# Kernel optimization log

Measured on AMD Instinct MI355X. Metric: run time of the kernel, lower is better.

The kernel has to match this reference:

```python
import jax, jax.numpy as jnp
import numpy as np

B, L, D = 4, 4096, 1024
H = 16
DK = D // H  # 64
EPS = 1e-5


def setup_inputs() -> dict:
    key = jax.random.key(0)
    ks = jax.random.split(key, 9)
    s = 1.0 / np.sqrt(D)
    return {
        "Q": jax.random.normal(ks[0], (B, L, D), dtype=jnp.float32),
        "W_Q": jax.random.uniform(ks[1], (D, D), jnp.float32, -s, s),
        "b_Q": jax.random.uniform(ks[2], (D,), jnp.float32, -s, s),
        "W_K": jax.random.uniform(ks[3], (D, D), jnp.float32, -s, s),
        "b_K": jax.random.uniform(ks[4], (D,), jnp.float32, -s, s),
        "W_V": jax.random.uniform(ks[5], (D, D), jnp.float32, -s, s),
        "b_V": jax.random.uniform(ks[6], (D,), jnp.float32, -s, s),
        "W_O": jax.random.uniform(ks[7], (D, D), jnp.float32, -s, s),
        "b_O": jax.random.uniform(ks[8], (D,), jnp.float32, -s, s),
    }


def reference(Q, W_Q, b_Q, W_K, b_K, W_V, b_V, W_O, b_O):
    # Projections (torch Linear: x @ W.T + b). K = V = Q (self-attention).
    q = (Q @ W_Q.T + b_Q).reshape(B, L, H, DK)  # blhd
    k = (Q @ W_K.T + b_K).reshape(B, L, H, DK)
    v = (Q @ W_V.T + b_V).reshape(B, L, H, DK)

    phi_q = jax.nn.elu(q) + 1.0
    phi_k = jax.nn.elu(k) + 1.0

    # KV outer-product accumulation over sequence: [b,h,d,m]
    KV = jnp.einsum('blhd,blhm->bhdm', phi_k, v)
    K_sum = phi_k.sum(axis=1)                       # [b,h,d]
    Z = 1.0 / (jnp.einsum('blhd,bhd->blh', phi_q, K_sum) + EPS)
    V_new = jnp.einsum('blhd,bhdm->blhm', phi_q, KV) * Z[..., None]

    out = V_new.reshape(B, L, H * DK) @ W_O.T + b_O  # [b,L,d_model]
    return out
```

## Files before the change

kernel.cpp:

```cpp
#include <hip/hip_runtime.h>

typedef unsigned short u16;
typedef unsigned int   u32;
typedef __attribute__((ext_vector_type(8))) short short8;
typedef __attribute__((ext_vector_type(4))) float f32x4;
typedef __attribute__((ext_vector_type(4))) u16   u16x4;

#define NB 4
#define SL 4096
#define DM 1024
#define NH 16
#define DK 64

__device__ __forceinline__ u16 f2bf(float f) {
  u32 u = __builtin_bit_cast(u32, f);
  u = (u + 0x7fffu + ((u >> 16) & 1u)) >> 16;
  return (u16)u;
}
__device__ __forceinline__ float bf2f(u16 v) {
  u32 u = ((u32)v) << 16;
  return __builtin_bit_cast(float, u);
}
__device__ __forceinline__ float eluP1(float x) {
  return x > 0.f ? x + 1.f : __expf(x);
}
#define GLL(gp, lp) __builtin_amdgcn_global_load_lds(     \
    (const __attribute__((address_space(1))) void*)(gp),  \
    (__attribute__((address_space(3))) void*)(lp), 16, 0, 0)

__global__ void cvt_all(const float* __restrict__ Qf,
                        const float* __restrict__ WQ, const float* __restrict__ WK,
                        const float* __restrict__ WV, const float* __restrict__ WO,
                        const float* __restrict__ bQ, const float* __restrict__ bK,
                        const float* __restrict__ bV,
                        u16* __restrict__ Qbf, u16* __restrict__ Wqkv,
                        u16* __restrict__ Wobf, float* __restrict__ biasQKV) {
  int b = blockIdx.x, tid = threadIdx.x;
  if (b < 16384) {
    int i = b * 256 + tid;
    f32x4 f = *(const f32x4*)(Qf + (size_t)i * 4);
    u16x4 o = { f2bf(f[0]), f2bf(f[1]), f2bf(f[2]), f2bf(f[3]) };
    *(u16x4*)(Qbf + (size_t)i * 4) = o;
  } else if (b < 20480) {
    int r = (b - 16384) >> 10;
    int i = ((b - 16384) & 1023) * 256 + tid;
    const float* src = r == 0 ? WQ : r == 1 ? WK : r == 2 ? WV : WO;
    u16* dst = (r == 3) ? Wobf : Wqkv + (size_t)r * 1048576;
    f32x4 f = *(const f32x4*)(src + (size_t)i * 4);
    u16x4 o = { f2bf(f[0]), f2bf(f[1]), f2bf(f[2]), f2bf(f[3]) };
    *(u16x4*)(dst + (size_t)i * 4) = o;
  } else {
    int i = (b - 20480) * 256 + tid;
    if (i < 3072) {
      float v = (i < 1024) ? bQ[i] : (i < 2048) ? bK[i - 1024] : bV[i - 2048];
      biasQKV[i] = v;
    }
  }
}


#define VM8 asm volatile("s_waitcnt vmcnt(8)" ::: "memory")
#define NOP ((void)0)

#define SA(buf, ks, kt) do {                                      \
    const u16* g_ = Ag + (((kt) & 15) * 64 + (ks) * 32);          \
    u16* l_ = ldsA + (buf) * 32768 + (ks) * 8192;                 \
    GLL(g_, l_); GLL(g_ + 16 * 1024, l_ + 512); } while (0)

#define SB(buf, ks, kt) do {                                      \
    const u16* g_ = Wg + (((kt) & 15) * 64 + (ks) * 32);          \
    u16* l_ = ldsB + (buf) * 32768 + (ks) * 8192;                 \
    GLL(g_, l_); GLL(g_ + 16 * 1024, l_ + 512); } while (0)

#define LDB(buf, ks) do {                                         \
    const u16* pB_ = bBase + (buf) * 32768 + (ks) * 8192;         \
    bf0 = *(const short8*)(pB_ + bOff[0]);                        \
    bf1 = *(const short8*)(pB_ + bOff[1]);                        \
    bf2 = *(const short8*)(pB_ + bOff[2]);                        \
    bf3 = *(const short8*)(pB_ + bOff[3]); } while (0)

#define PHASE(buf, ks, tb, PRE, STG) do {                         \
    short8 af_[4];                                                \
    const u16* pA_ = aBase + (buf) * 32768 + (ks) * 8192;         \
    _Pragma("unroll") for (int t_ = 0; t_ < 4; t_++)              \
      af_[t_] = *(const short8*)(pA_ + aOff[(tb) + t_]);          \
    PRE;                                                          \
    STG;                                                          \
    VM8;                                                          \
    __builtin_amdgcn_s_barrier();                                 \
    asm volatile("s_waitcnt lgkmcnt(0)" ::: "memory");            \
    __builtin_amdgcn_s_setprio(1);                                \
    _Pragma("unroll") for (int t_ = 0; t_ < 4; t_++) {            \
      acc[(tb) + t_][0] = __builtin_amdgcn_mfma_f32_16x16x32_bf16(af_[t_], bf0, acc[(tb) + t_][0], 0, 0, 0); \
      acc[(tb) + t_][1] = __builtin_amdgcn_mfma_f32_16x16x32_bf16(af_[t_], bf1, acc[(tb) + t_][1], 0, 0, 0); \
      acc[(tb) + t_][2] = __builtin_amdgcn_mfma_f32_16x16x32_bf16(af_[t_], bf2, acc[(tb) + t_][2], 0, 0, 0); \
      acc[(tb) + t_][3] = __builtin_amdgcn_mfma_f32_16x16x32_bf16(af_[t_], bf3, acc[(tb) + t_][3], 0, 0, 0); \
    }                                                             \
    __builtin_amdgcn_s_setprio(0);                                \
  } while (0)

#define MAIN_8PHASE_LOOP                                          \
  SA(0, 0, 0); SB(0, 0, 0); SA(0, 1, 0); SB(0, 1, 0);             \
  SA(1, 0, 1); SB(1, 0, 1);                                       \
  VM8;                                                            \
  __builtin_amdgcn_s_barrier();                                   \
  asm volatile("" ::: "memory");                                  \
  _Pragma("unroll 1")                                             \
  for (int i = 0; i < 8; i++) {                                   \
    PHASE(0, 0, 0, LDB(0, 0), SB(1, 1, 2 * i + 1));               \
    PHASE(0, 0, 4, NOP,       SA(1, 1, 2 * i + 1));               \
    PHASE(0, 1, 0, LDB(0, 1), SB(0, 0, 2 * i + 2));               \
    PHASE(0, 1, 4, NOP,       SA(0, 0, 2 * i + 2));               \
    PHASE(1, 0, 0, LDB(1, 0), SB(0, 1, 2 * i + 2));               \
    PHASE(1, 0, 4, NOP,       SA(0, 1, 2 * i + 2));               \
    PHASE(1, 1, 0, LDB(1, 1), SB(1, 0, 2 * i + 3));               \
    PHASE(1, 1, 4, NOP,       SA(1, 0, 2 * i + 3));               \
  }

__global__ __launch_bounds__(512, 2) void gemm_qkv(const u16* __restrict__ A,
                                                   const u16* __restrict__ Wqkv,
                                                   const float* __restrict__ biasQKV,
                                                   u16* __restrict__ phiq,
                                                   u16* __restrict__ phiKT,
                                                   u16* __restrict__ vT) {
  const int K = 1024;
  const int bId = blockIdx.x;
  const int xcd = bId & 7, s = bId >> 3;
  const int tile_m = xcd * 8 + s / 12;
  const int tile_n = s % 12;
  const int region = tile_n >> 2;

  const int tid = threadIdx.x, lane = tid & 63, wv = tid >> 6;
  const int i16 = lane & 15, q = lane >> 4;
  const int waveM = wv >> 2, waveN = wv & 3;

  __shared__ u16 smem[65536];

  const int r0 = wv * 32 + (lane >> 2);
  const int kc = (lane & 3) ^ ((r0 >> 1) & 3);
  const u16* Ag = A + (size_t)(tile_m * 256 + r0) * K + kc * 8;
  const u16* Wg = Wqkv + (size_t)(tile_n * 256 + r0) * K + kc * 8;
  u16* ldsA = smem + wv * 1024;
  u16* ldsB = smem + 16384 + wv * 1024;

  const u16* aBase = (region == 0) ? smem + 16384 : smem;
  const u16* bBase = (region == 0) ? smem : smem + 16384;
  int aOff[8], bOff[4];
#pragma unroll
  for (int t = 0; t < 8; t++) {
    int m = waveM * 128 + t * 16 + i16;
    aOff[t] = m * 32 + ((q ^ ((m >> 1) & 3)) << 3);
  }
#pragma unroll
  for (int u = 0; u < 4; u++) {
    int n = waveN * 64 + u * 16 + i16;
    bOff[u] = n * 32 + ((q ^ ((n >> 1) & 3)) << 3);
  }

  f32x4 acc[8][4] = {};
  short8 bf0, bf1, bf2, bf3;

  MAIN_8PHASE_LOOP

  u16* T = smem;
  const int TS = 132;
  u16* dstT = (region == 1) ? phiKT : vT;
  const int bI = tile_m >> 4;
  const int lb = (tile_m & 15) * 256;

#pragma unroll
  for (int h = 0; h < 2; h++) {
    __syncthreads();
    if (waveM == h) {
      if (region == 0) {
#pragma unroll
        for (int t = 0; t < 8; t++) {
          f32x4 b4 = *(const f32x4*)(biasQKV + tile_n * 256 + h * 128 + t * 16 + q * 4);
#pragma unroll
          for (int u = 0; u < 4; u++) {
            int cC = waveN * 64 + u * 16 + i16;
            u16x4 o;
#pragma unroll
            for (int r = 0; r < 4; r++) o[r] = f2bf(eluP1(acc[t][u][r] + b4[r]));
            *(u16x4*)(T + cC * TS + t * 16 + q * 4) = o;
          }
        }
      } else {
#pragma unroll
        for (int u = 0; u < 4; u++) {
          int cC = waveN * 64 + u * 16 + i16;
          float bs = biasQKV[tile_n * 256 + cC];
#pragma unroll
          for (int t = 0; t < 8; t++) {
            u16x4 o;
#pragma unroll
            for (int r = 0; r < 4; r++) {
              float vv = acc[t][u][r] + bs;
              if (region == 1) vv = eluP1(vv);
              o[r] = f2bf(vv);
            }
            *(u16x4*)(T + cC * TS + t * 16 + q * 4) = o;
          }
        }
      }
    }
    __syncthreads();
    {
      const int Rl = tid >> 4, c16 = (tid & 15) * 8;
#pragma unroll
      for (int p = 0; p < 8; p++) {
        int R = p * 32 + Rl;
        short8 v8 = *(const short8*)(T + R * TS + c16);
        if (region == 0) {
          *(short8*)(phiq + (size_t)(tile_m * 256 + R) * DM + tile_n * 256 + h * 128 + c16) = v8;
        } else {
          int n_loc = tile_n * 256 + R - region * 1024;
          *(short8*)(dstT + ((size_t)bI * 1024 + n_loc) * 4096 + lb + h * 128 + c16) = v8;
        }
      }
    }
  }
}

__global__ __launch_bounds__(512, 2) void gemm_out(const u16* __restrict__ A,
                                                   const u16* __restrict__ W,
                                                   const float* __restrict__ bias,
                                                   float* __restrict__ outp) {
  const int K = 1024;
  const int bId = blockIdx.x;
  const int xcd = bId & 7, s = bId >> 3;
  const int tile_m = xcd * 8 + (s >> 2);
  const int tile_n = s & 3;

  const int tid = threadIdx.x, lane = tid & 63, wv = tid >> 6;
  const int i16 = lane & 15, q = lane >> 4;
  const int waveM = wv >> 2, waveN = wv & 3;

  __shared__ u16 smem[65536];

  const int r0 = wv * 32 + (lane >> 2);
  const int kc = (lane & 3) ^ ((r0 >> 1) & 3);
  const u16* Ag = A + (size_t)(tile_m * 256 + r0) * K + kc * 8;
  const u16* Wg = W + (size_t)(tile_n * 256 + r0) * K + kc * 8;
  u16* ldsA = smem + wv * 1024;
  u16* ldsB = smem + 16384 + wv * 1024;

  const u16* aBase = smem + 16384;
  const u16* bBase = smem;
  int aOff[8], bOff[4];
#pragma unroll
  for (int t = 0; t < 8; t++) {
    int m = waveM * 128 + t * 16 + i16;
    aOff[t] = m * 32 + ((q ^ ((m >> 1) & 3)) << 3);
  }
#pragma unroll
  for (int u = 0; u < 4; u++) {
    int n = waveN * 64 + u * 16 + i16;
    bOff[u] = n * 32 + ((q ^ ((n >> 1) & 3)) << 3);
  }

  f32x4 acc[8][4] = {};
  short8 bf0, bf1, bf2, bf3;

  MAIN_8PHASE_LOOP

  float* Tf = (float*)smem;
  const int TFS = 68;
#pragma unroll
  for (int qn = 0; qn < 4; qn++) {
    __syncthreads();
    if (waveM == (qn >> 1)) {
      const int tb = (qn & 1) * 4;
#pragma unroll
      for (int tt = 0; tt < 4; tt++) {
        f32x4 b4 = *(const f32x4*)(bias + tile_n * 256 + qn * 64 + tt * 16 + q * 4);
#pragma unroll
        for (int u = 0; u < 4; u++) {
          int l = waveN * 64 + u * 16 + i16;
          f32x4 o;
#pragma unroll
          for (int r = 0; r < 4; r++) o[r] = acc[tb + tt][u][r] + b4[r];
          *(f32x4*)(Tf + l * TFS + tt * 16 + q * 4) = o;
        }
      }
    }
    __syncthreads();
    {
      const int Rl = tid >> 4, j = tid & 15;
#pragma unroll
      for (int p = 0; p < 8; p++) {
        int R = p * 32 + Rl;
        f32x4 v = *(const f32x4*)(Tf + R * TFS + j * 4);
        *(f32x4*)(outp + (size_t)(tile_m * 256 + R) * DM + tile_n * 256 + qn * 64 + j * 4) = v;
      }
    }
  }
}

__global__ __launch_bounds__(256) void kv_partial(const u16* __restrict__ phiKT,
                                                  const u16* __restrict__ vT,
                                                  float* __restrict__ part,
                                                  float* __restrict__ ksumP) {
  int bh = blockIdx.x >> 2, chunk = blockIdx.x & 3;
  int tid = threadIdx.x, lane = tid & 63, wv = tid >> 6;
  int i16 = lane & 15, q = lane >> 4;
  const u16* Ab = phiKT + (size_t)bh * DK * SL;
  const u16* Bb = vT + (size_t)bh * DK * SL;
  int l0 = (chunk * 4 + wv) * 256;
  f32x4 acc[4][4] = {};
  float ks[4] = {};
  for (int kk = 0; kk < 256; kk += 32) {
    int col = l0 + kk + q * 8;
    short8 af[4], bfr[4];
#pragma unroll
    for (int t = 0; t < 4; t++) af[t] = *(const short8*)(Ab + (size_t)(t * 16 + i16) * SL + col);
#pragma unroll
    for (int u = 0; u < 4; u++) bfr[u] = *(const short8*)(Bb + (size_t)(u * 16 + i16) * SL + col);
#pragma unroll
    for (int t = 0; t < 4; t++)
#pragma unroll
      for (int j = 0; j < 8; j++) ks[t] += bf2f((u16)af[t][j]);
#pragma unroll
    for (int t = 0; t < 4; t++)
#pragma unroll
      for (int u = 0; u < 4; u++)
        acc[t][u] = __builtin_amdgcn_mfma_f32_16x16x32_bf16(af[t], bfr[u], acc[t][u], 0, 0, 0);
  }
  __shared__ float red[4][64][64];
  __shared__ float ksl[4][4][64];
#pragma unroll
  for (int t = 0; t < 4; t++)
#pragma unroll
    for (int u = 0; u < 4; u++)
#pragma unroll
      for (int r = 0; r < 4; r++)
        red[wv][t * 16 + q * 4 + r][u * 16 + i16] = acc[t][u][r];
#pragma unroll
  for (int t = 0; t < 4; t++) ksl[wv][q][t * 16 + i16] = ks[t];
  __syncthreads();
  int d = tid >> 2, mg = (tid & 3) * 16;
#pragma unroll
  for (int c = 0; c < 4; c++) {
    int m = mg + c * 4;
    f32x4 o;
#pragma unroll
    for (int r = 0; r < 4; r++)
      o[r] = red[0][d][m + r] + red[1][d][m + r] + red[2][d][m + r] + red[3][d][m + r];
    *(f32x4*)(part + ((size_t)(chunk * 64 + bh) * 64 + d) * 64 + m) = o;
  }
  if (tid < 64) {
    float s = 0.f;
#pragma unroll
    for (int w2 = 0; w2 < 4; w2++)
#pragma unroll
      for (int q2 = 0; q2 < 4; q2++) s += ksl[w2][q2][tid];
    ksumP[chunk * 4096 + bh * 64 + tid] = s;
  }
}

__global__ __launch_bounds__(256) void kv_finalize(const float* __restrict__ part,
                                                   const float* __restrict__ ksumP,
                                                   u16* __restrict__ KVt,
                                                   float* __restrict__ Ksum) {
  int bh = blockIdx.x, tid = threadIdx.x;
  for (int e = tid; e < 4096; e += 256) {
    int d = e >> 6, m = e & 63;
    float s = part[((size_t)(0 * 64 + bh) * 64 + d) * 64 + m]
            + part[((size_t)(1 * 64 + bh) * 64 + d) * 64 + m]
            + part[((size_t)(2 * 64 + bh) * 64 + d) * 64 + m]
            + part[((size_t)(3 * 64 + bh) * 64 + d) * 64 + m];
    KVt[(size_t)bh * 4096 + m * 64 + d] = f2bf(s);
  }
  if (tid < 64) {
    float s = ksumP[0 * 4096 + bh * 64 + tid] + ksumP[1 * 4096 + bh * 64 + tid]
            + ksumP[2 * 4096 + bh * 64 + tid] + ksumP[3 * 4096 + bh * 64 + tid];
    Ksum[bh * 64 + tid] = s;
  }
}

__global__ __launch_bounds__(256) void vnew_kernel(const u16* __restrict__ phiq,
                                                   const u16* __restrict__ KVt,
                                                   const float* __restrict__ Ksum,
                                                   u16* __restrict__ Vnew) {
  int bh = blockIdx.x >> 5, lt = blockIdx.x & 31;
  int b = bh >> 4, h = bh & 15;
  int tid = threadIdx.x, lane = tid & 63, wv = tid >> 6;
  int i16 = lane & 15, q = lane >> 4;
  int waveM = wv & 1, waveL = wv >> 1;

  __shared__ u16 T[128 * 72];

  f32x4 ks00 = *(const f32x4*)(Ksum + bh * 64 + q * 8);
  f32x4 ks01 = *(const f32x4*)(Ksum + bh * 64 + q * 8 + 4);
  f32x4 ks10 = *(const f32x4*)(Ksum + bh * 64 + 32 + q * 8);
  f32x4 ks11 = *(const f32x4*)(Ksum + bh * 64 + 32 + q * 8 + 4);

  f32x4 acc[2][4] = {};
  float zp[4] = {0.f, 0.f, 0.f, 0.f};
#pragma unroll
  for (int step = 0; step < 2; step++) {
    int d0 = step * 32 + q * 8;
    short8 af[2], bfr[4];
#pragma unroll
    for (int t = 0; t < 2; t++) {
      int m = waveM * 32 + t * 16 + i16;
      af[t] = *(const short8*)(KVt + (size_t)bh * 4096 + m * 64 + d0);
    }
#pragma unroll
    for (int u = 0; u < 4; u++) {
      int l = lt * 128 + waveL * 64 + u * 16 + i16;
      bfr[u] = *(const short8*)(phiq + (size_t)(b * SL + l) * DM + h * 64 + d0);
      f32x4 k0 = step == 0 ? ks00 : ks10;
      f32x4 k1 = step == 0 ? ks01 : ks11;
#pragma unroll
      for (int j = 0; j < 4; j++) zp[u] += bf2f((u16)bfr[u][j]) * k0[j];
#pragma unroll
      for (int j = 0; j < 4; j++) zp[u] += bf2f((u16)bfr[u][4 + j]) * k1[j];
    }
#pragma unroll
    for (int t = 0; t < 2; t++)
#pragma unroll
      for (int u = 0; u < 4; u++)
        acc[t][u] = __builtin_amdgcn_mfma_f32_16x16x32_bf16(af[t], bfr[u], acc[t][u], 0, 0, 0);
  }

  float z[4];
#pragma unroll
  for (int u = 0; u < 4; u++) {
    float s = zp[u];
    s += __shfl_xor(s, 16);
    s += __shfl_xor(s, 32);
    z[u] = 1.0f / (s + 1e-5f);
  }

#pragma unroll
  for (int t = 0; t < 2; t++) {
#pragma unroll
    for (int u = 0; u < 4; u++) {
      int cI = waveL * 64 + u * 16 + i16;
      int nI = waveM * 32 + t * 16 + q * 4;
      u16x4 o;
#pragma unroll
      for (int r = 0; r < 4; r++) o[r] = f2bf(acc[t][u][r] * z[u]);
      *(u16x4*)(T + cI * 72 + nI) = o;
    }
  }
  __syncthreads();
  {
    const int Rl = tid >> 3, j = tid & 7;
#pragma unroll
    for (int p = 0; p < 4; p++) {
      int R = p * 32 + Rl;
      short8 v8 = *(const short8*)(T + R * 72 + j * 8);
      *(short8*)(Vnew + (size_t)(b * SL + lt * 128 + R) * DM + h * 64 + j * 8) = v8;
    }
  }
}

extern "C" void kernel_launch(void* const* d_in, const int* in_sizes, int n_in,
                              void* d_out, int out_size, void* d_ws, size_t ws_size,
                              hipStream_t stream) {
  const float* Qf = (const float*)d_in[0];
  const float* WQ = (const float*)d_in[1];
  const float* bQ = (const float*)d_in[2];
  const float* WK = (const float*)d_in[3];
  const float* bK = (const float*)d_in[4];
  const float* WV = (const float*)d_in[5];
  const float* bV = (const float*)d_in[6];
  const float* WO = (const float*)d_in[7];
  const float* bO = (const float*)d_in[8];

  const size_t MB = 1024ull * 1024ull;
  char* ws = (char*)d_ws;
  u16* Qbf     = (u16*)(ws + 0);
  u16* Vnew    = (u16*)(ws + 0);
  u16* Wqkv    = (u16*)(ws + 32 * MB);
  u16* Wobf    = (u16*)(ws + 38 * MB);
  float* biasQKV = (float*)(ws + 40 * MB);
  u16* phiq    = (u16*)(ws + 41 * MB);
  u16* phiKT   = (u16*)(ws + 73 * MB);
  u16* vT      = (u16*)(ws + 105 * MB);
  u16* KVt     = (u16*)(ws + 137 * MB);
  float* Ksum  = (float*)(ws + 138 * MB);
  float* part  = (float*)(ws + 139 * MB);
  float* ksumP = (float*)(ws + 143 * MB);

  cvt_all<<<20492, 256, 0, stream>>>(Qf, WQ, WK, WV, WO, bQ, bK, bV,
                                     Qbf, Wqkv, Wobf, biasQKV);

  gemm_qkv<<<768, 512, 0, stream>>>(Qbf, Wqkv, biasQKV, phiq, phiKT, vT);

  kv_partial<<<256, 256, 0, stream>>>(phiKT, vT, part, ksumP);
  kv_finalize<<<64, 256, 0, stream>>>(part, ksumP, KVt, Ksum);

  vnew_kernel<<<2048, 256, 0, stream>>>(phiq, KVt, Ksum, Vnew);

  gemm_out<<<256, 512, 0, stream>>>(Vnew, Wobf, bO, (float*)d_out);
}
```

Before: 328.9 us.

## Double-buffer LDS fragment reads across phases to overlap with MFMA

Restructures the 8-phase GEMM main loop so the LDS fragment reads for the next phase are issued before the current phase's MFMAs. Two register sets each are used for A and B fragments, and a partial lgkmcnt wait replaces the full wait. The barrier and global-to-LDS staging now sit after the MFMAs, and the stage order is shifted, with SB(1,1) moved into the prologue. This aims to hide LDS read latency behind matrix math, at the cost of more registers and a subtler buffer-reuse ordering that could race if the waits are wrong.

```diff
diff --git a/kernel.cpp b/kernel.cpp
--- a/kernel.cpp
+++ b/kernel.cpp
@@ -60,7 +60,6 @@
 
 
 #define VM8 asm volatile("s_waitcnt vmcnt(8)" ::: "memory")
-#define NOP ((void)0)
 
 #define SA(buf, ks, kt) do {                                      \
     const u16* g_ = Ag + (((kt) & 15) * 64 + (ks) * 32);          \
@@ -72,49 +71,57 @@
     u16* l_ = ldsB + (buf) * 32768 + (ks) * 8192;                 \
     GLL(g_, l_); GLL(g_ + 16 * 1024, l_ + 512); } while (0)
 
-#define LDB(buf, ks) do {                                         \
-    const u16* pB_ = bBase + (buf) * 32768 + (ks) * 8192;         \
-    bf0 = *(const short8*)(pB_ + bOff[0]);                        \
-    bf1 = *(const short8*)(pB_ + bOff[1]);                        \
-    bf2 = *(const short8*)(pB_ + bOff[2]);                        \
-    bf3 = *(const short8*)(pB_ + bOff[3]); } while (0)
-
-#define PHASE(buf, ks, tb, PRE, STG) do {                         \
-    short8 af_[4];                                                \
+#define RD4(SET, buf, ks) do {                                    \
     const u16* pA_ = aBase + (buf) * 32768 + (ks) * 8192;         \
     _Pragma("unroll") for (int t_ = 0; t_ < 4; t_++)              \
-      af_[t_] = *(const short8*)(pA_ + aOff[(tb) + t_]);          \
-    PRE;                                                          \
+      SET[t_] = *(const short8*)(pA_ + aOff[4 + t_]); } while (0)
+
+#define RD8(ASET, BSET, buf, ks) do {                             \
+    const u16* pA_ = aBase + (buf) * 32768 + (ks) * 8192;         \
+    const u16* pB_ = bBase + (buf) * 32768 + (ks) * 8192;         \
+    _Pragma("unroll") for (int t_ = 0; t_ < 4; t_++)              \
+      ASET[t_] = *(const short8*)(pA_ + aOff[t_]);                \
+    _Pragma("unroll") for (int u_ = 0; u_ < 4; u_++)              \
+      BSET[u_] = *(const short8*)(pB_ + bOff[u_]); } while (0)
+
+#define MFMA16(AF, BF, tb)                                        \
+    _Pragma("unroll") for (int t_ = 0; t_ < 4; t_++) {            \
+      acc[(tb) + t_][0] = __builtin_amdgcn_mfma_f32_16x16x32_bf16(AF[t_], BF[0], acc[(tb) + t_][0], 0, 0, 0); \
+      acc[(tb) + t_][1] = __builtin_amdgcn_mfma_f32_16x16x32_bf16(AF[t_], BF[1], acc[(tb) + t_][1], 0, 0, 0); \
+      acc[(tb) + t_][2] = __builtin_amdgcn_mfma_f32_16x16x32_bf16(AF[t_], BF[2], acc[(tb) + t_][2], 0, 0, 0); \
+      acc[(tb) + t_][3] = __builtin_amdgcn_mfma_f32_16x16x32_bf16(AF[t_], BF[3], acc[(tb) + t_][3], 0, 0, 0); \
+    }
+
+#define PH(AFC, BFC, tb, RDOP, N, STG) do {                       \
+    RDOP;                                                         \
+    asm volatile("s_waitcnt lgkmcnt(" #N ")" ::: "memory");       \
+    __builtin_amdgcn_sched_barrier(0);                            \
+    __builtin_amdgcn_s_setprio(1);                                \
+    MFMA16(AFC, BFC, tb);                                         \
+    __builtin_amdgcn_s_setprio(0);                                \
     STG;                                                          \
     VM8;                                                          \
     __builtin_amdgcn_s_barrier();                                 \
-    asm volatile("s_waitcnt lgkmcnt(0)" ::: "memory");            \
-    __builtin_amdgcn_s_setprio(1);                                \
-    _Pragma("unroll") for (int t_ = 0; t_ < 4; t_++) {            \
-      acc[(tb) + t_][0] = __builtin_amdgcn_mfma_f32_16x16x32_bf16(af_[t_], bf0, acc[(tb) + t_][0], 0, 0, 0); \
-      acc[(tb) + t_][1] = __builtin_amdgcn_mfma_f32_16x16x32_bf16(af_[t_], bf1, acc[(tb) + t_][1], 0, 0, 0); \
-      acc[(tb) + t_][2] = __builtin_amdgcn_mfma_f32_16x16x32_bf16(af_[t_], bf2, acc[(tb) + t_][2], 0, 0, 0); \
-      acc[(tb) + t_][3] = __builtin_amdgcn_mfma_f32_16x16x32_bf16(af_[t_], bf3, acc[(tb) + t_][3], 0, 0, 0); \
-    }                                                             \
-    __builtin_amdgcn_s_setprio(0);                                \
   } while (0)
 
 #define MAIN_8PHASE_LOOP                                          \
+  short8 afA[4], afB[4], bfX[4], bfY[4];                          \
   SA(0, 0, 0); SB(0, 0, 0); SA(0, 1, 0); SB(0, 1, 0);             \
-  SA(1, 0, 1); SB(1, 0, 1);                                       \
+  SA(1, 0, 1); SB(1, 0, 1); SB(1, 1, 1);                          \
   VM8;                                                            \
   __builtin_amdgcn_s_barrier();                                   \
   asm volatile("" ::: "memory");                                  \
+  RD8(afA, bfX, 0, 0);                                            \
   _Pragma("unroll 1")                                             \
   for (int i = 0; i < 8; i++) {                                   \
-    PHASE(0, 0, 0, LDB(0, 0), SB(1, 1, 2 * i + 1));               \
-    PHASE(0, 0, 4, NOP,       SA(1, 1, 2 * i + 1));               \
-    PHASE(0, 1, 0, LDB(0, 1), SB(0, 0, 2 * i + 2));               \
-    PHASE(0, 1, 4, NOP,       SA(0, 0, 2 * i + 2));               \
-    PHASE(1, 0, 0, LDB(1, 0), SB(0, 1, 2 * i + 2));               \
-    PHASE(1, 0, 4, NOP,       SA(0, 1, 2 * i + 2));               \
-    PHASE(1, 1, 0, LDB(1, 1), SB(1, 0, 2 * i + 3));               \
-    PHASE(1, 1, 4, NOP,       SA(1, 0, 2 * i + 3));               \
+    PH(afA, bfX, 0, RD4(afB, 0, 0),        4, SA(1, 1, 2 * i + 1)); \
+    PH(afB, bfX, 4, RD8(afA, bfY, 0, 1),   8, SB(0, 0, 2 * i + 2)); \
+    PH(afA, bfY, 0, RD4(afB, 0, 1),        4, SA(0, 0, 2 * i + 2)); \
+    PH(afB, bfY, 4, RD8(afA, bfX, 1, 0),   8, SB(0, 1, 2 * i + 2)); \
+    PH(afA, bfX, 0, RD4(afB, 1, 0),        4, SA(0, 1, 2 * i + 2)); \
+    PH(afB, bfX, 4, RD8(afA, bfY, 1, 1),   8, SB(1, 0, 2 * i + 3)); \
+    PH(afA, bfY, 0, RD4(afB, 1, 1),        4, SA(1, 0, 2 * i + 3)); \
+    PH(afB, bfY, 4, RD8(afA, bfX, 0, 0),   8, SB(1, 1, 2 * i + 3)); \
   }
 
 __global__ __launch_bounds__(512, 2) void gemm_qkv(const u16* __restrict__ A,
@@ -158,7 +165,6 @@
   }
 
   f32x4 acc[8][4] = {};
-  short8 bf0, bf1, bf2, bf3;
 
   MAIN_8PHASE_LOOP
 
@@ -260,7 +266,6 @@
   }
 
   f32x4 acc[8][4] = {};
-  short8 bf0, bf1, bf2, bf3;
 
   MAIN_8PHASE_LOOP
 
```

After: 334.2 us. No clear change (+1.6%).

## Replace gemm_out 8-phase pipeline with a 4-slot LDS ring buffer

Applied to the files above, without the earlier changes.

Rewrites the main loop of the output-projection GEMM as a 4-deep LDS ring of K=32 slices. Each iteration stages two slices ahead, computes two slices, then waits on vmcnt(0) and a single barrier, instead of using a barrier per phase. The A and B LDS regions are resized to hold four slots each. The aim is to cut barrier and phase-coordination overhead, at the cost of a full memory drain on each iteration, which may expose load latency. The old 8-phase macros are renamed but still used by the QKV GEMM.

```diff
diff --git a/kernel.cpp b/kernel.cpp
--- a/kernel.cpp
+++ b/kernel.cpp
@@ -60,26 +60,26 @@
 
 
 #define VM8 asm volatile("s_waitcnt vmcnt(8)" ::: "memory")
-#define NOP ((void)0)
-
-#define SA(buf, ks, kt) do {                                      \
+#define NOP8 ((void)0)
+
+#define SA8(buf, ks, kt) do {                                     \
     const u16* g_ = Ag + (((kt) & 15) * 64 + (ks) * 32);          \
     u16* l_ = ldsA + (buf) * 32768 + (ks) * 8192;                 \
     GLL(g_, l_); GLL(g_ + 16 * 1024, l_ + 512); } while (0)
 
-#define SB(buf, ks, kt) do {                                      \
+#define SB8(buf, ks, kt) do {                                     \
     const u16* g_ = Wg + (((kt) & 15) * 64 + (ks) * 32);          \
     u16* l_ = ldsB + (buf) * 32768 + (ks) * 8192;                 \
     GLL(g_, l_); GLL(g_ + 16 * 1024, l_ + 512); } while (0)
 
-#define LDB(buf, ks) do {                                         \
+#define LDB8(buf, ks) do {                                        \
     const u16* pB_ = bBase + (buf) * 32768 + (ks) * 8192;         \
     bf0 = *(const short8*)(pB_ + bOff[0]);                        \
     bf1 = *(const short8*)(pB_ + bOff[1]);                        \
     bf2 = *(const short8*)(pB_ + bOff[2]);                        \
     bf3 = *(const short8*)(pB_ + bOff[3]); } while (0)
 
-#define PHASE(buf, ks, tb, PRE, STG) do {                         \
+#define PHASE8(buf, ks, tb, PRE, STG) do {                        \
     short8 af_[4];                                                \
     const u16* pA_ = aBase + (buf) * 32768 + (ks) * 8192;         \
     _Pragma("unroll") for (int t_ = 0; t_ < 4; t_++)              \
@@ -100,21 +100,21 @@
   } while (0)
 
 #define MAIN_8PHASE_LOOP                                          \
-  SA(0, 0, 0); SB(0, 0, 0); SA(0, 1, 0); SB(0, 1, 0);             \
-  SA(1, 0, 1); SB(1, 0, 1);                                       \
+  SA8(0, 0, 0); SB8(0, 0, 0); SA8(0, 1, 0); SB8(0, 1, 0);         \
+  SA8(1, 0, 1); SB8(1, 0, 1);                                     \
   VM8;                                                            \
   __builtin_amdgcn_s_barrier();                                   \
   asm volatile("" ::: "memory");                                  \
   _Pragma("unroll 1")                                             \
   for (int i = 0; i < 8; i++) {                                   \
-    PHASE(0, 0, 0, LDB(0, 0), SB(1, 1, 2 * i + 1));               \
-    PHASE(0, 0, 4, NOP,       SA(1, 1, 2 * i + 1));               \
-    PHASE(0, 1, 0, LDB(0, 1), SB(0, 0, 2 * i + 2));               \
-    PHASE(0, 1, 4, NOP,       SA(0, 0, 2 * i + 2));               \
-    PHASE(1, 0, 0, LDB(1, 0), SB(0, 1, 2 * i + 2));               \
-    PHASE(1, 0, 4, NOP,       SA(0, 1, 2 * i + 2));               \
-    PHASE(1, 1, 0, LDB(1, 1), SB(1, 0, 2 * i + 3));               \
-    PHASE(1, 1, 4, NOP,       SA(1, 0, 2 * i + 3));               \
+    PHASE8(0, 0, 0, LDB8(0, 0), SB8(1, 1, 2 * i + 1));            \
+    PHASE8(0, 0, 4, NOP8,       SA8(1, 1, 2 * i + 1));            \
+    PHASE8(0, 1, 0, LDB8(0, 1), SB8(0, 0, 2 * i + 2));            \
+    PHASE8(0, 1, 4, NOP8,       SA8(0, 0, 2 * i + 2));            \
+    PHASE8(1, 0, 0, LDB8(1, 0), SB8(0, 1, 2 * i + 2));            \
+    PHASE8(1, 0, 4, NOP8,       SA8(0, 1, 2 * i + 2));            \
+    PHASE8(1, 1, 0, LDB8(1, 1), SB8(1, 0, 2 * i + 3));            \
+    PHASE8(1, 1, 4, NOP8,       SA8(1, 0, 2 * i + 3));            \
   }
 
 __global__ __launch_bounds__(512, 2) void gemm_qkv(const u16* __restrict__ A,
@@ -222,6 +222,61 @@
   }
 }
 
+
+#define VM0R asm volatile("s_waitcnt vmcnt(0)" ::: "memory")
+
+#define SAR(kt) do {                                              \
+    const u16* g_ = Ag + (((kt) & 31) * 32);                      \
+    u16* l_ = ldsA + (((kt) & 3) * 8192);                         \
+    GLL(g_, l_); GLL(g_ + 16 * 1024, l_ + 512); } while (0)
+
+#define SBR(kt) do {                                              \
+    const u16* g_ = Wg + (((kt) & 31) * 32);                      \
+    u16* l_ = ldsB + (((kt) & 3) * 8192);                         \
+    GLL(g_, l_); GLL(g_ + 16 * 1024, l_ + 512); } while (0)
+
+#define STG2R(kt) do { SAR(kt); SBR(kt); } while (0)
+
+#define MFMA16R(AF, BF, tb)                                       \
+    _Pragma("unroll") for (int t_ = 0; t_ < 4; t_++) {            \
+      acc[(tb) + t_][0] = __builtin_amdgcn_mfma_f32_16x16x32_bf16(AF[t_], BF[0], acc[(tb) + t_][0], 0, 0, 0); \
+      acc[(tb) + t_][1] = __builtin_amdgcn_mfma_f32_16x16x32_bf16(AF[t_], BF[1], acc[(tb) + t_][1], 0, 0, 0); \
+      acc[(tb) + t_][2] = __builtin_amdgcn_mfma_f32_16x16x32_bf16(AF[t_], BF[2], acc[(tb) + t_][2], 0, 0, 0); \
+      acc[(tb) + t_][3] = __builtin_amdgcn_mfma_f32_16x16x32_bf16(AF[t_], BF[3], acc[(tb) + t_][3], 0, 0, 0); \
+    }
+
+#define TILER(buf) do {                                           \
+    short8 a0_[4], b_[4];                                         \
+    _Pragma("unroll") for (int t_ = 0; t_ < 4; t_++)              \
+      a0_[t_] = *(const short8*)(aBase + (buf) * 8192 + aOff[t_]);\
+    _Pragma("unroll") for (int u_ = 0; u_ < 4; u_++)              \
+      b_[u_] = *(const short8*)(bBase + (buf) * 8192 + bOff[u_]); \
+    __builtin_amdgcn_s_setprio(1);                                \
+    MFMA16R(a0_, b_, 0);                                          \
+    __builtin_amdgcn_s_setprio(0);                                \
+    short8 a4_[4];                                                \
+    _Pragma("unroll") for (int t_ = 0; t_ < 4; t_++)              \
+      a4_[t_] = *(const short8*)(aBase + (buf) * 8192 + aOff[4 + t_]); \
+    __builtin_amdgcn_s_setprio(1);                                \
+    MFMA16R(a4_, b_, 4);                                          \
+    __builtin_amdgcn_s_setprio(0);                                \
+  } while (0)
+
+#define MAIN_RING_LOOP                                            \
+  STG2R(0); STG2R(1);                                             \
+  VM0R;                                                           \
+  __builtin_amdgcn_s_barrier();                                   \
+  asm volatile("" ::: "memory");                                  \
+  _Pragma("unroll 1")                                             \
+  for (int kt = 0; kt < 32; kt += 2) {                            \
+    STG2R(kt + 2);                                                \
+    TILER(kt & 3);                                                \
+    STG2R(kt + 3);                                                \
+    TILER((kt + 1) & 3);                                          \
+    VM0R;                                                         \
+    __builtin_amdgcn_s_barrier();                                 \
+  }
+
 __global__ __launch_bounds__(512, 2) void gemm_out(const u16* __restrict__ A,
                                                    const u16* __restrict__ W,
                                                    const float* __restrict__ bias,
@@ -243,9 +298,9 @@
   const u16* Ag = A + (size_t)(tile_m * 256 + r0) * K + kc * 8;
   const u16* Wg = W + (size_t)(tile_n * 256 + r0) * K + kc * 8;
   u16* ldsA = smem + wv * 1024;
-  u16* ldsB = smem + 16384 + wv * 1024;
-
-  const u16* aBase = smem + 16384;
+  u16* ldsB = smem + 32768 + wv * 1024;
+
+  const u16* aBase = smem + 32768;
   const u16* bBase = smem;
   int aOff[8], bOff[4];
 #pragma unroll
@@ -260,9 +315,8 @@
   }
 
   f32x4 acc[8][4] = {};
-  short8 bf0, bf1, bf2, bf3;
-
-  MAIN_8PHASE_LOOP
+
+  MAIN_RING_LOOP
 
   float* Tf = (float*)smem;
   const int TFS = 68;
```

After: 332.6 us. Within noise of the previous version (+1.1%).
